# Kernel tuning notes

Hardware: AMD Instinct MI355X
Metric: run time of the kernel (lower is better)

## Reference

```python
import jax, jax.numpy as jnp
import numpy as np

DIM, NUM_HEADS, WINDOW = 1024, 16, 256
HEAD_DIM = DIM // NUM_HEADS
B, L = 2, 2048


def rotate_half(x):
    x1, x2 = jnp.split(x, 2, axis=-1)
    return jnp.concatenate([-x2, x1], axis=-1)


def setup_inputs() -> dict:
    key = jax.random.key(0)
    kx, kq, kk, kv, ko = jax.random.split(key, 5)
    x = jax.random.normal(kx, (B, L, DIM), dtype=jnp.float32)
    # realistic RoPE tables (L, head_dim)
    inv_freq = 1.0 / (10000.0 ** (np.arange(0, HEAD_DIM, 2, dtype=np.float32) / HEAD_DIM))
    ang = np.arange(L, dtype=np.float32)[:, None] * inv_freq[None, :]  # (L, hd/2)
    ang = np.concatenate([ang, ang], axis=-1)  # (L, hd)
    cos = jnp.asarray(np.cos(ang))
    sin = jnp.asarray(np.sin(ang))
    scale = 1.0 / np.sqrt(DIM)
    Wq = jax.random.normal(kq, (DIM, DIM), dtype=jnp.float32) * scale
    Wk = jax.random.normal(kk, (DIM, DIM), dtype=jnp.float32) * scale
    Wv = jax.random.normal(kv, (DIM, DIM), dtype=jnp.float32) * scale
    Wo = jax.random.normal(ko, (DIM, DIM), dtype=jnp.float32) * scale
    return {"x": x, "cos": cos, "sin": sin, "Wq": Wq, "Wk": Wk, "Wv": Wv, "Wo": Wo}


def reference(x, cos, sin, Wq, Wk, Wv, Wo):
    Bx, Lx, D = x.shape
    H, hd, w = NUM_HEADS, HEAD_DIM, WINDOW
    q = (x @ Wq.T).reshape(Bx, Lx, H, hd)
    k = (x @ Wk.T).reshape(Bx, Lx, H, hd)
    v = (x @ Wv.T).reshape(Bx, Lx, H, hd)
    c = cos[None, :, None, :]  # broadcast over batch, heads
    s = sin[None, :, None, :]
    q = q * c + rotate_half(q) * s
    k = k * c + rotate_half(k) * s
    # (B, H, L, hd)
    q = q.transpose(0, 2, 1, 3)
    k = k.transpose(0, 2, 1, 3)
    v = v.transpose(0, 2, 1, 3)
    i = jnp.arange(Lx)[:, None]
    j = jnp.arange(Lx)[None, :]
    # causal & within sliding window: i - w <= j <= i
    mask = (j <= i) & (j >= i - w)
    scores = jnp.einsum("bhqd,bhkd->bhqk", q, k) / jnp.sqrt(jnp.asarray(hd, x.dtype))
    scores = jnp.where(mask[None, None], scores, jnp.finfo(scores.dtype).min)
    attn = jax.nn.softmax(scores, axis=-1)
    out = jnp.einsum("bhqk,bhkd->bhqd", attn, v)
    out = out.transpose(0, 2, 1, 3).reshape(Bx, Lx, D)
    return out @ Wo.T
```

## Files before the change

### kernel.cpp

```cpp
#include <hip/hip_runtime.h>

#define DIM 1024
#define NH  16
#define HD  64
#define BB  2
#define LL  2048
#define WIN 256
#define MM  (BB * LL)
#define NQKV (3 * DIM)
#define SEG  (DIM * DIM)

typedef __bf16 bf16x8 __attribute__((ext_vector_type(8)));
typedef float  f32x4  __attribute__((ext_vector_type(4)));
typedef unsigned short u16x8 __attribute__((ext_vector_type(8)));

__device__ __forceinline__ unsigned short f2bf(float f) {
    union { float f; unsigned int i; } v; v.f = f;
    unsigned int r = v.i + 0x7fffu + ((v.i >> 16) & 1u);
    return (unsigned short)(r >> 16);
}
__device__ __forceinline__ bf16x8 load8bf(const unsigned short* p) {
    uint4 u = *reinterpret_cast<const uint4*>(p);
    return __builtin_bit_cast(bf16x8, u);
}
__device__ __forceinline__ void gll16(const void* g, void* l) {
    __builtin_amdgcn_global_load_lds(
        (const __attribute__((address_space(1))) unsigned int*)g,
        (__attribute__((address_space(3))) unsigned int*)l, 16, 0, 0);
}

__global__ __launch_bounds__(256) void convert_inputs(
    const float* __restrict__ x,
    const float* __restrict__ Wq, const float* __restrict__ Wk,
    const float* __restrict__ Wv, const float* __restrict__ Wo,
    unsigned short* __restrict__ xb,
    unsigned short* __restrict__ wqkv,
    unsigned short* __restrict__ wob)
{
    const int y = blockIdx.y;
    const size_t base = ((size_t)blockIdx.x * 256 + threadIdx.x) * 8;
    const float* src; unsigned short* dst;
    if (y < 4)       { src = x + (size_t)y * SEG;  dst = xb + (size_t)y * SEG; }
    else if (y == 4) { src = Wq; dst = wqkv; }
    else if (y == 5) { src = Wk; dst = wqkv + SEG; }
    else if (y == 6) { src = Wv; dst = wqkv + 2 * (size_t)SEG; }
    else             { src = Wo; dst = wob; }
    float4 a = ((const float4*)(src + base))[0];
    float4 b = ((const float4*)(src + base))[1];
    u16x8 r;
    r[0] = f2bf(a.x); r[1] = f2bf(a.y); r[2] = f2bf(a.z); r[3] = f2bf(a.w);
    r[4] = f2bf(b.x); r[5] = f2bf(b.y); r[6] = f2bf(b.z); r[7] = f2bf(b.w);
    *(u16x8*)(dst + base) = r;
}

__global__ __launch_bounds__(256, 4) void qkv_gemm(
    const unsigned short* __restrict__ xb,
    const unsigned short* __restrict__ wqkv,
    const float* __restrict__ cosb, const float* __restrict__ sinb,
    unsigned short* __restrict__ qws, unsigned short* __restrict__ kws,
    unsigned short* __restrict__ vT)
{
    __shared__ __align__(16) unsigned short smem[2 * 128 * 64];
    unsigned short* As = smem;
    unsigned short* Bs = smem + 128 * 64;
    const int t = threadIdx.x;
    const int lane = t & 63, w = t >> 6;
    const int wm = w >> 1, wn = w & 1;
    const int lr = lane & 15, quad = lane >> 4;

    const int id   = blockIdx.y * 24 + blockIdx.x;
    const int xcd  = id & 7, slot = id >> 3;
    const int bxn  = (xcd & 1) * 12 + (slot % 12);
    const int byn  = (xcd >> 1) * 8 + (slot / 12);
    const int n0 = bxn * 128, m0 = byn * 128;

    f32x4 acc[4][4];
    for (int i = 0; i < 4; i++) for (int j = 0; j < 4; j++) acc[i][j] = 0.0f;

    const int rsub = t >> 3;
    const int csw  = (t & 7) ^ (rsub & 7);
    const int sw7  = lr & 7;

    for (int k0 = 0; k0 < DIM; k0 += 64) {
        __syncthreads();
        #pragma unroll
        for (int p = 0; p < 4; p++) {
            const int row = p * 32 + rsub;
            gll16(xb   + (size_t)(m0 + row) * DIM + k0 + csw * 8,
                  &As[p * 2048 + t * 8]);
            gll16(wqkv + (size_t)(n0 + row) * DIM + k0 + csw * 8,
                  &Bs[p * 2048 + t * 8]);
        }
        __syncthreads();
        #pragma unroll
        for (int kk = 0; kk < 2; kk++) {
            bf16x8 af[4], bfr[4];
            #pragma unroll
            for (int mi = 0; mi < 4; mi++) {
                const int R = wm * 64 + mi * 16 + lr;
                af[mi] = load8bf(&As[R * 64 + (((kk * 4 + quad) ^ sw7) * 8)]);
            }
            #pragma unroll
            for (int ni = 0; ni < 4; ni++) {
                const int R = wn * 64 + ni * 16 + lr;
                bfr[ni] = load8bf(&Bs[R * 64 + (((kk * 4 + quad) ^ sw7) * 8)]);
            }
            #pragma unroll
            for (int mi = 0; mi < 4; mi++)
                #pragma unroll
                for (int ni = 0; ni < 4; ni++)
                    acc[mi][ni] = __builtin_amdgcn_mfma_f32_16x16x32_bf16(
                        af[mi], bfr[ni], acc[mi][ni], 0, 0, 0);
        }
    }

    const int ng = n0 + wn * 64;
    const int which = ng >> 10;
    const int h = (ng & (DIM - 1)) >> 6;

    if (which == 2) {
        __syncthreads();
        unsigned short* T = smem + w * 2048;
        const int token0 = m0 + wm * 64;
        const int b  = token0 >> 11;
        const int lg = (token0 & (LL - 1)) + (lane & 7) * 8;
        #pragma unroll
        for (int p = 0; p < 2; p++) {
            #pragma unroll
            for (int ni = 2 * p; ni < 2 * p + 2; ni++) {
                const int dl = (ni & 1) * 16 + lr;
                const int g4 = (dl & 7) << 2;
                #pragma unroll
                for (int mi = 0; mi < 4; mi++)
                    #pragma unroll
                    for (int reg = 0; reg < 4; reg++) {
                        const int l = mi * 16 + quad * 4 + reg;
                        const int cw = (l >> 1) ^ g4;
                        T[dl * 64 + cw * 2 + (l & 1)] = f2bf(acc[mi][ni][reg]);
                    }
            }
            #pragma unroll
            for (int s = 0; s < 4; s++) {
                const int dl = s * 8 + (lane >> 3);
                const int d  = p * 32 + dl;
                const int g4 = (dl & 7) << 2;
                const int pd = ((lane & 7) * 4) ^ g4;
                uint4 val = *(const uint4*)&T[dl * 64 + pd * 2];
                *(uint4*)&vT[((size_t)(b * NH + h) * HD + d) * LL + lg] = val;
            }
        }
    } else {
        unsigned short* dst = (which == 0) ? qws : kws;
        #pragma unroll
        for (int mi = 0; mi < 4; mi++) {
            #pragma unroll
            for (int reg = 0; reg < 4; reg++) {
                const int row = m0 + wm * 64 + mi * 16 + quad * 4 + reg;
                const int b = row >> 11, l = row & (LL - 1);
                #pragma unroll
                for (int ni = 0; ni < 4; ni++) {
                    const int d = ni * 16 + lr;
                    const float c = cosb[l * HD + d];
                    const float s = sinb[l * HD + d];
                    const float partner = (d < 32) ? -acc[mi][ni + 2][reg]
                                                   :  acc[mi][ni - 2][reg];
                    dst[((size_t)(b * NH + h) * LL + l) * HD + d] =
                        f2bf(acc[mi][ni][reg] * c + partner * s);
                }
            }
        }
    }
}

#define PSTR 40
__global__ __launch_bounds__(256, 4) void swa_attn(
    const unsigned short* __restrict__ qws,
    const unsigned short* __restrict__ kws,
    const unsigned short* __restrict__ vT,
    unsigned short* __restrict__ aout)
{
    __shared__ __align__(16) unsigned short Pc[4][16][PSTR];

    const int t = threadIdx.x;
    const int lane = t & 63, w = t >> 6;

    const int id   = (blockIdx.z * 16 + blockIdx.y) * 32 + blockIdx.x;
    const int xcd  = id & 7, slot = id >> 3;
    const int hb   = xcd * 4 + (slot >> 5);
    const int qb   = slot & 31;
    const int h = hb & 15, b = hb >> 4;

    const int q0 = qb * 64;

    const int lr = lane & 15, quad = lane >> 4, ko = quad * 8;
    const size_t base = ((size_t)(b * NH + h)) * LL * HD;
    const unsigned short* Q  = qws + base;
    const unsigned short* K  = kws + base;
    const unsigned short* VT = vT + base;

    const int i0 = q0 + w * 16;
    const int wkey = i0 - WIN;
    const bf16x8 qa0 = load8bf(Q + (size_t)(i0 + lr) * HD + ko);
    const bf16x8 qa1 = load8bf(Q + (size_t)(i0 + lr) * HD + 32 + ko);

    float rowsum[4] = {0.f, 0.f, 0.f, 0.f};
    f32x4 o[4];
    #pragma unroll
    for (int nt = 0; nt < 4; nt++) o[nt] = 0.0f;

    if (q0 >= WIN) {
        bool mlo[4], mhi[4];
        #pragma unroll
        for (int reg = 0; reg < 4; reg++) {
            mlo[reg] = (lr >= quad * 4 + reg);
            mhi[reg] = (lr <= quad * 4 + reg);
        }
        #pragma unroll
        for (int kc = 0; kc < 9; kc++) {
            {
                const int kt = 2 * kc;
                const int jr = wkey + kt * 16 + lr;
                const bf16x8 kb0 = load8bf(K + (size_t)jr * HD + ko);
                const bf16x8 kb1 = load8bf(K + (size_t)jr * HD + 32 + ko);
                f32x4 s = 0.0f;
                s = __builtin_amdgcn_mfma_f32_16x16x32_bf16(qa0, kb0, s, 0, 0, 0);
                s = __builtin_amdgcn_mfma_f32_16x16x32_bf16(qa1, kb1, s, 0, 0, 0);
                #pragma unroll
                for (int reg = 0; reg < 4; reg++) {
                    float e = __expf(s[reg] * 0.125f);
                    if (kt == 0)  e = mlo[reg] ? e : 0.0f;
                    if (kt == 16) e = mhi[reg] ? e : 0.0f;
                    rowsum[reg] += e;
                    Pc[w][quad * 4 + reg][lr] = f2bf(e);
                }
            }
            bf16x8 bv[4];
            {
                int kb = wkey + kc * 32 + ko;
                kb = min(kb, LL - 8);
                #pragma unroll
                for (int nt = 0; nt < 4; nt++)
                    bv[nt] = load8bf(VT + (size_t)(nt * 16 + lr) * LL + kb);
            }
            {
                const int kt = 2 * kc + 1;
                if (kt > 16) {
                    #pragma unroll
                    for (int reg = 0; reg < 4; reg++)
                        Pc[w][quad * 4 + reg][16 + lr] = 0;
                } else {
                    const int jr = wkey + kt * 16 + lr;
                    const bf16x8 kb0 = load8bf(K + (size_t)jr * HD + ko);
                    const bf16x8 kb1 = load8bf(K + (size_t)jr * HD + 32 + ko);
                    f32x4 s = 0.0f;
                    s = __builtin_amdgcn_mfma_f32_16x16x32_bf16(qa0, kb0, s, 0, 0, 0);
                    s = __builtin_amdgcn_mfma_f32_16x16x32_bf16(qa1, kb1, s, 0, 0, 0);
                    #pragma unroll
                    for (int reg = 0; reg < 4; reg++) {
                        const float e = __expf(s[reg] * 0.125f);
                        rowsum[reg] += e;
                        Pc[w][quad * 4 + reg][16 + lr] = f2bf(e);
                    }
                }
            }
            const bf16x8 pa = load8bf(&Pc[w][lr][ko]);
            #pragma unroll
            for (int nt = 0; nt < 4; nt++)
                o[nt] = __builtin_amdgcn_mfma_f32_16x16x32_bf16(pa, bv[nt], o[nt], 0, 0, 0);
        }
    } else {
        #pragma unroll
        for (int kc = 0; kc < 9; kc++) {
            #pragma unroll
            for (int sub = 0; sub < 2; sub++) {
                const int kt = 2 * kc + sub;
                const int j  = wkey + kt * 16 + lr;
                const int jc = min(max(j, 0), LL - 1);
                const bf16x8 kb0 = load8bf(K + (size_t)jc * HD + ko);
                const bf16x8 kb1 = load8bf(K + (size_t)jc * HD + 32 + ko);
                f32x4 s = 0.0f;
                s = __builtin_amdgcn_mfma_f32_16x16x32_bf16(qa0, kb0, s, 0, 0, 0);
                s = __builtin_amdgcn_mfma_f32_16x16x32_bf16(qa1, kb1, s, 0, 0, 0);
                #pragma unroll
                for (int reg = 0; reg < 4; reg++) {
                    const int i = i0 + quad * 4 + reg;
                    const bool valid = (j >= 0) && (j <= i) && (j >= i - WIN);
                    const float e = valid ? __expf(s[reg] * 0.125f) : 0.0f;
                    rowsum[reg] += e;
                    Pc[w][quad * 4 + reg][sub * 16 + lr] = f2bf(e);
                }
            }
            const bf16x8 pa = load8bf(&Pc[w][lr][ko]);
            int kb = wkey + kc * 32 + ko;
            kb = min(max(kb, 0), LL - 8);
            bf16x8 bv[4];
            #pragma unroll
            for (int nt = 0; nt < 4; nt++)
                bv[nt] = load8bf(VT + (size_t)(nt * 16 + lr) * LL + kb);
            #pragma unroll
            for (int nt = 0; nt < 4; nt++)
                o[nt] = __builtin_amdgcn_mfma_f32_16x16x32_bf16(pa, bv[nt], o[nt], 0, 0, 0);
        }
    }

    float inv[4];
    #pragma unroll
    for (int reg = 0; reg < 4; reg++) {
        float s = rowsum[reg];
        s += __shfl_xor(s, 1); s += __shfl_xor(s, 2);
        s += __shfl_xor(s, 4); s += __shfl_xor(s, 8);
        inv[reg] = 1.0f / s;
    }

    #pragma unroll
    for (int nt = 0; nt < 4; nt++) {
        #pragma unroll
        for (int reg = 0; reg < 4; reg++) {
            const int i = i0 + quad * 4 + reg;
            const int d = nt * 16 + lr;
            aout[((size_t)(b * LL + i)) * DIM + h * HD + d] =
                f2bf(o[nt][reg] * inv[reg]);
        }
    }
}

__global__ __launch_bounds__(256, 4) void out_gemm(
    const unsigned short* __restrict__ A,
    const unsigned short* __restrict__ Wob,
    float* __restrict__ out)
{
    __shared__ __align__(16) unsigned short smem[64 * 64 + 64 * 64];
    unsigned short* As = smem;
    unsigned short* Bs = smem + 64 * 64;
    const int t = threadIdx.x;
    const int lane = t & 63, w = t >> 6;
    const int wm = w >> 1, wn = w & 1;
    const int lr = lane & 15, quad = lane >> 4;

    const int id   = blockIdx.y * 16 + blockIdx.x;
    const int xcd  = id & 7, slot = id >> 3;
    const int bx   = (xcd & 1) * 8 + (slot & 7);
    const int by   = (xcd >> 1) * 16 + (slot >> 3);
    const int n0 = bx * 64, m0 = by * 64;

    f32x4 acc[2][2];
    for (int i = 0; i < 2; i++) for (int j = 0; j < 2; j++) acc[i][j] = 0.0f;

    const int rsub = t >> 3;
    const int csw  = (t & 7) ^ (rsub & 7);
    const int sw7  = lr & 7;

    for (int k0 = 0; k0 < DIM; k0 += 64) {
        __syncthreads();
        #pragma unroll
        for (int p = 0; p < 2; p++) {
            const int row = p * 32 + rsub;
            gll16(A   + (size_t)(m0 + row) * DIM + k0 + csw * 8,
                  &As[p * 2048 + t * 8]);
            gll16(Wob + (size_t)(n0 + row) * DIM + k0 + csw * 8,
                  &Bs[p * 2048 + t * 8]);
        }
        __syncthreads();
        #pragma unroll
        for (int kk = 0; kk < 2; kk++) {
            bf16x8 af[2], bfr[2];
            #pragma unroll
            for (int mi = 0; mi < 2; mi++) {
                const int R = wm * 32 + mi * 16 + lr;
                af[mi] = load8bf(&As[R * 64 + (((kk * 4 + quad) ^ sw7) * 8)]);
            }
            #pragma unroll
            for (int ni = 0; ni < 2; ni++) {
                const int R = wn * 32 + ni * 16 + lr;
                bfr[ni] = load8bf(&Bs[R * 64 + (((kk * 4 + quad) ^ sw7) * 8)]);
            }
            #pragma unroll
            for (int mi = 0; mi < 2; mi++)
                #pragma unroll
                for (int ni = 0; ni < 2; ni++)
                    acc[mi][ni] = __builtin_amdgcn_mfma_f32_16x16x32_bf16(
                        af[mi], bfr[ni], acc[mi][ni], 0, 0, 0);
        }
    }

    #pragma unroll
    for (int mi = 0; mi < 2; mi++) {
        #pragma unroll
        for (int reg = 0; reg < 4; reg++) {
            const int row = m0 + wm * 32 + mi * 16 + quad * 4 + reg;
            #pragma unroll
            for (int ni = 0; ni < 2; ni++) {
                const int col = n0 + wn * 32 + ni * 16 + lr;
                out[(size_t)row * DIM + col] = acc[mi][ni][reg];
            }
        }
    }
}

extern "C" void kernel_launch(void* const* d_in, const int* in_sizes, int n_in,
                              void* d_out, int out_size, void* d_ws, size_t ws_size,
                              hipStream_t stream)
{
    const float* x    = (const float*)d_in[0];
    const float* cosb = (const float*)d_in[1];
    const float* sinb = (const float*)d_in[2];
    const float* Wq   = (const float*)d_in[3];
    const float* Wk   = (const float*)d_in[4];
    const float* Wv   = (const float*)d_in[5];
    const float* Wo   = (const float*)d_in[6];
    float* out = (float*)d_out;

    unsigned short* xb   = (unsigned short*)d_ws;
    unsigned short* wqkv = xb + (size_t)MM * DIM;
    unsigned short* wob  = wqkv + (size_t)NQKV * DIM;
    unsigned short* qws  = wob + (size_t)DIM * DIM;
    unsigned short* kws  = qws + (size_t)BB * NH * LL * HD;
    unsigned short* vT   = kws + (size_t)BB * NH * LL * HD;
    unsigned short* aws  = xb;

    convert_inputs<<<dim3(SEG / (256 * 8), 8), 256, 0, stream>>>(
        x, Wq, Wk, Wv, Wo, xb, wqkv, wob);
    qkv_gemm<<<dim3(NQKV / 128, MM / 128), 256, 0, stream>>>(
        xb, wqkv, cosb, sinb, qws, kws, vT);
    swa_attn<<<dim3(LL / 64, NH, BB), 256, 0, stream>>>(qws, kws, vT, aws);
    out_gemm<<<dim3(DIM / 64, MM / 64), 256, 0, stream>>>(aws, wob, out);
}
```

Baseline: 165.0 us.

## Stage sliding-window K tile in swizzled LDS shared by 8 waves

The attention kernel now processes 128 query rows per block with 512 threads and cooperatively loads the 384-row key span into LDS once, using an XOR swizzle. All eight waves then read K from LDS instead of each issuing its own global loads, which removes redundant global K traffic across overlapping windows. The P scratch buffer is double-buffered per wave. In exchange, LDS use per block grows and a block barrier is added, which may lower occupancy; V is still read from global memory.

```diff
diff --git a/kernel.cpp b/kernel.cpp
--- a/kernel.cpp
+++ b/kernel.cpp
@@ -172,25 +172,28 @@
     }
 }
 
+#define SW_SPAN 384
 #define PSTR 40
-__global__ __launch_bounds__(256, 4) void swa_attn(
+__global__ __launch_bounds__(512, 4) void swa_attn(
     const unsigned short* __restrict__ qws,
     const unsigned short* __restrict__ kws,
     const unsigned short* __restrict__ vT,
     unsigned short* __restrict__ aout)
 {
-    __shared__ __align__(16) unsigned short Pc[4][16][PSTR];
+    __shared__ __align__(16) unsigned short Ks[SW_SPAN * 64];
+    __shared__ __align__(16) unsigned short Pc[8][2][16][PSTR];
 
     const int t = threadIdx.x;
     const int lane = t & 63, w = t >> 6;
 
-    const int id   = (blockIdx.z * 16 + blockIdx.y) * 32 + blockIdx.x;
+    const int id   = (blockIdx.z * NH + blockIdx.y) * 16 + blockIdx.x;
     const int xcd  = id & 7, slot = id >> 3;
-    const int hb   = xcd * 4 + (slot >> 5);
-    const int qb   = slot & 31;
+    const int hb   = xcd * 4 + (slot >> 4);
+    const int qb   = slot & 15;
     const int h = hb & 15, b = hb >> 4;
 
-    const int q0 = qb * 64;
+    const int q0 = qb * 128;
+    const int base_key = q0 - WIN;
 
     const int lr = lane & 15, quad = lane >> 4, ko = quad * 8;
     const size_t base = ((size_t)(b * NH + h)) * LL * HD;
@@ -198,10 +201,20 @@
     const unsigned short* K  = kws + base;
     const unsigned short* VT = vT + base;
 
+    {
+        const int rsub = t >> 3;
+        const int csw  = (t & 7) ^ (rsub & 7);
+        #pragma unroll
+        for (int p = 0; p < 6; p++) {
+            const int j = min(max(base_key + p * 64 + rsub, 0), LL - 1);
+            gll16(K + (size_t)j * HD + csw * 8, &Ks[p * 4096 + t * 8]);
+        }
+    }
     const int i0 = q0 + w * 16;
     const int wkey = i0 - WIN;
     const bf16x8 qa0 = load8bf(Q + (size_t)(i0 + lr) * HD + ko);
     const bf16x8 qa1 = load8bf(Q + (size_t)(i0 + lr) * HD + 32 + ko);
+    __syncthreads();
 
     float rowsum[4] = {0.f, 0.f, 0.f, 0.f};
     f32x4 o[4];
@@ -217,11 +230,12 @@
         }
         #pragma unroll
         for (int kc = 0; kc < 9; kc++) {
+            const int pb = kc & 1;
             {
                 const int kt = 2 * kc;
-                const int jr = wkey + kt * 16 + lr;
-                const bf16x8 kb0 = load8bf(K + (size_t)jr * HD + ko);
-                const bf16x8 kb1 = load8bf(K + (size_t)jr * HD + 32 + ko);
+                const int R = w * 16 + kt * 16 + lr;
+                const bf16x8 kb0 = load8bf(&Ks[R * 64 + ((quad       ^ (R & 7)) * 8)]);
+                const bf16x8 kb1 = load8bf(&Ks[R * 64 + (((quad + 4) ^ (R & 7)) * 8)]);
                 f32x4 s = 0.0f;
                 s = __builtin_amdgcn_mfma_f32_16x16x32_bf16(qa0, kb0, s, 0, 0, 0);
                 s = __builtin_amdgcn_mfma_f32_16x16x32_bf16(qa1, kb1, s, 0, 0, 0);
@@ -231,7 +245,7 @@
                     if (kt == 0)  e = mlo[reg] ? e : 0.0f;
                     if (kt == 16) e = mhi[reg] ? e : 0.0f;
                     rowsum[reg] += e;
-                    Pc[w][quad * 4 + reg][lr] = f2bf(e);
+                    Pc[w][pb][quad * 4 + reg][lr] = f2bf(e);
                 }
             }
             bf16x8 bv[4];
@@ -247,11 +261,11 @@
                 if (kt > 16) {
                     #pragma unroll
                     for (int reg = 0; reg < 4; reg++)
-                        Pc[w][quad * 4 + reg][16 + lr] = 0;
+                        Pc[w][pb][quad * 4 + reg][16 + lr] = 0;
                 } else {
-                    const int jr = wkey + kt * 16 + lr;
-                    const bf16x8 kb0 = load8bf(K + (size_t)jr * HD + ko);
-                    const bf16x8 kb1 = load8bf(K + (size_t)jr * HD + 32 + ko);
+                    const int R = w * 16 + kt * 16 + lr;
+                    const bf16x8 kb0 = load8bf(&Ks[R * 64 + ((quad       ^ (R & 7)) * 8)]);
+                    const bf16x8 kb1 = load8bf(&Ks[R * 64 + (((quad + 4) ^ (R & 7)) * 8)]);
                     f32x4 s = 0.0f;
                     s = __builtin_amdgcn_mfma_f32_16x16x32_bf16(qa0, kb0, s, 0, 0, 0);
                     s = __builtin_amdgcn_mfma_f32_16x16x32_bf16(qa1, kb1, s, 0, 0, 0);
@@ -259,11 +273,11 @@
                     for (int reg = 0; reg < 4; reg++) {
                         const float e = __expf(s[reg] * 0.125f);
                         rowsum[reg] += e;
-                        Pc[w][quad * 4 + reg][16 + lr] = f2bf(e);
+                        Pc[w][pb][quad * 4 + reg][16 + lr] = f2bf(e);
                     }
                 }
             }
-            const bf16x8 pa = load8bf(&Pc[w][lr][ko]);
+            const bf16x8 pa = load8bf(&Pc[w][pb][lr][ko]);
             #pragma unroll
             for (int nt = 0; nt < 4; nt++)
                 o[nt] = __builtin_amdgcn_mfma_f32_16x16x32_bf16(pa, bv[nt], o[nt], 0, 0, 0);
@@ -271,26 +285,27 @@
     } else {
         #pragma unroll
         for (int kc = 0; kc < 9; kc++) {
+            const int pb = kc & 1;
             #pragma unroll
             for (int sub = 0; sub < 2; sub++) {
                 const int kt = 2 * kc + sub;
-                const int j  = wkey + kt * 16 + lr;
-                const int jc = min(max(j, 0), LL - 1);
-                const bf16x8 kb0 = load8bf(K + (size_t)jc * HD + ko);
-                const bf16x8 kb1 = load8bf(K + (size_t)jc * HD + 32 + ko);
+                const int R = min(w * 16 + kt * 16 + lr, SW_SPAN - 1);
+                const bf16x8 kb0 = load8bf(&Ks[R * 64 + ((quad       ^ (R & 7)) * 8)]);
+                const bf16x8 kb1 = load8bf(&Ks[R * 64 + (((quad + 4) ^ (R & 7)) * 8)]);
                 f32x4 s = 0.0f;
                 s = __builtin_amdgcn_mfma_f32_16x16x32_bf16(qa0, kb0, s, 0, 0, 0);
                 s = __builtin_amdgcn_mfma_f32_16x16x32_bf16(qa1, kb1, s, 0, 0, 0);
                 #pragma unroll
                 for (int reg = 0; reg < 4; reg++) {
                     const int i = i0 + quad * 4 + reg;
+                    const int j = wkey + kt * 16 + lr;
                     const bool valid = (j >= 0) && (j <= i) && (j >= i - WIN);
                     const float e = valid ? __expf(s[reg] * 0.125f) : 0.0f;
                     rowsum[reg] += e;
-                    Pc[w][quad * 4 + reg][sub * 16 + lr] = f2bf(e);
+                    Pc[w][pb][quad * 4 + reg][sub * 16 + lr] = f2bf(e);
                 }
             }
-            const bf16x8 pa = load8bf(&Pc[w][lr][ko]);
+            const bf16x8 pa = load8bf(&Pc[w][pb][lr][ko]);
             int kb = wkey + kc * 32 + ko;
             kb = min(max(kb, 0), LL - 8);
             bf16x8 bv[4];
@@ -422,6 +437,6 @@
         x, Wq, Wk, Wv, Wo, xb, wqkv, wob);
     qkv_gemm<<<dim3(NQKV / 128, MM / 128), 256, 0, stream>>>(
         xb, wqkv, cosb, sinb, qws, kws, vT);
-    swa_attn<<<dim3(LL / 64, NH, BB), 256, 0, stream>>>(qws, kws, vT, aws);
+    swa_attn<<<dim3(LL / 128, NH, BB), 512, 0, stream>>>(qws, kws, vT, aws);
     out_gemm<<<dim3(DIM / 64, MM / 64), 256, 0, stream>>>(aws, wob, out);
 }
```

Result: faster. 157.6 us (-4.5%).
